# Optimization experiments

Measured on AMD Instinct MI355X. Metric: run time of the kernel, lower is better.

## Reference

```python
import jax, jax.numpy as jnp
import numpy as np

BN_EPS = 1e-5


def setup_inputs() -> dict:
    key = jax.random.key(0)
    ks = jax.random.split(key, 12)
    N, E, H, INV = 100000, 500000, 128, 16
    DIN = 2 * H + INV  # 272
    x_send = jax.random.normal(ks[0], (N, H), dtype=jnp.float32)
    x_rec = jax.random.normal(ks[1], (N, H), dtype=jnp.float32)
    index = jax.random.randint(ks[2], (2, E), 0, N, dtype=jnp.int64)
    edge_attr = jax.random.normal(ks[3], (E, INV), dtype=jnp.float32)
    # message_mlp = BatchNorm1d(272) -> Linear(272,128) -> SiLU  (eval-mode BN)
    bn_gamma = jax.random.normal(ks[4], (DIN,), dtype=jnp.float32) * 0.1 + 1.0
    bn_beta = jax.random.normal(ks[5], (DIN,), dtype=jnp.float32) * 0.1
    bn_mean = jax.random.normal(ks[6], (DIN,), dtype=jnp.float32) * 0.1
    bn_var = jax.random.uniform(ks[7], (DIN,), dtype=jnp.float32) + 0.5
    W1 = jax.random.normal(ks[8], (DIN, H), dtype=jnp.float32) / np.sqrt(DIN)
    b1 = jnp.zeros((H,), dtype=jnp.float32)
    # edge_inf_mlp = Linear(128,1) -> Sigmoid
    W2 = jax.random.normal(ks[9], (H, 1), dtype=jnp.float32) / np.sqrt(H)
    b2 = jnp.zeros((1,), dtype=jnp.float32)
    return {"x_send": x_send, "x_rec": x_rec, "index": index, "edge_attr": edge_attr,
            "bn_gamma": bn_gamma, "bn_beta": bn_beta, "bn_mean": bn_mean, "bn_var": bn_var,
            "W1": W1, "b1": b1, "W2": W2, "b2": b2}


def reference(x_send, x_rec, index, edge_attr, bn_gamma, bn_beta, bn_mean, bn_var, W1, b1, W2, b2):
    idx_send, idx_rec = index[0], index[1]
    # gather + concat -> [E, 2H + INV]
    state = jnp.concatenate((x_send[idx_send], x_rec[idx_rec], edge_attr), axis=1)
    # eval-mode BatchNorm1d
    state = (state - bn_mean) * (bn_gamma * jax.lax.rsqrt(bn_var + BN_EPS)) + bn_beta
    # Linear + SiLU
    messages = jax.nn.silu(state @ W1 + b1)  # [E, H]
    # edge gating: Linear(H,1) + Sigmoid
    edge_weights = jax.nn.sigmoid(messages @ W2 + b2)  # [E, 1]
    # scatter_add aggregation over receiving nodes
    return jax.ops.segment_sum(messages * edge_weights, idx_rec, num_segments=x_rec.shape[0])
```

## Files before the change

kernel.cpp:

```cpp
#include <hip/hip_runtime.h>
#include <hip/hip_bf16.h>
#include <hip/hip_fp16.h>
#include <math.h>

#define HDIM 128
#define INVD 16
#define DIN 272
#define NKT 9

typedef __attribute__((ext_vector_type(4))) float f32x4;
typedef __attribute__((ext_vector_type(4))) unsigned u32x4;
typedef __attribute__((ext_vector_type(8))) short bf16x8;
typedef __attribute__((ext_vector_type(2))) __fp16 fp16x2;

__device__ inline short f2bf(float f) {
    union { float f; unsigned u; } v; v.f = f;
    unsigned r = v.u + 0x7FFFu + ((v.u >> 16) & 1u);
    return (short)(r >> 16);
}

__device__ inline unsigned cvt_pk_bf16(float a, float b) {
    unsigned r;
    asm("v_cvt_pk_bf16_f32 %0, %1, %2" : "=v"(r) : "v"(a), "v"(b));
    return r;
}

__device__ inline float fast_rcp(float x) {
    float r;
    asm("v_rcp_f32 %0, %1" : "=v"(r) : "v"(x));
    return r;
}

__global__ __launch_bounds__(256) void tobf16_kernel(const float* __restrict__ in,
                                                     unsigned short* __restrict__ o,
                                                     int n) {
    int i = (blockIdx.x * 256 + threadIdx.x) * 8;
    if (i < n) {
        f32x4 a = *(const f32x4*)(in + i);
        f32x4 b = *(const f32x4*)(in + i + 4);
        u32x4 r;
        r[0] = cvt_pk_bf16(a[0], a[1]);
        r[1] = cvt_pk_bf16(a[2], a[3]);
        r[2] = cvt_pk_bf16(b[0], b[1]);
        r[3] = cvt_pk_bf16(b[2], b[3]);
        *(u32x4*)(o + i) = r;
    }
}

template<int MODE>
__global__ __launch_bounds__(256, 2) void etnn_kernel(
    const float* __restrict__ x_send,
    const float* __restrict__ x_rec,
    const int*   __restrict__ index,
    const float* __restrict__ edge_attr,
    const float* __restrict__ bn_gamma,
    const float* __restrict__ bn_beta,
    const float* __restrict__ bn_mean,
    const float* __restrict__ bn_var,
    const float* __restrict__ W1,
    const float* __restrict__ b1,
    const float* __restrict__ W2,
    const float* __restrict__ b2,
    const unsigned short* __restrict__ xsb,
    const unsigned short* __restrict__ xrb,
    float* __restrict__ out,
    __half* __restrict__ ws,
    int E, int nIter)
{
    __shared__ short btab[NKT * 8 * 64 * 8];
    __shared__ float scl[DIN];
    __shared__ float shf[DIN];
    __shared__ float bias2[2][HDIM];
    __shared__ float biasT[HDIM];

    const int tid = threadIdx.x;
    const int l  = tid & 63;
    const int lr = l & 15;
    const int lg = l >> 4;

    for (int c = tid; c < DIN; c += 256) {
        float sc = bn_gamma[c] * rsqrtf(bn_var[c] + 1e-5f);
        scl[c] = sc;
        shf[c] = bn_beta[c] - bn_mean[c] * sc;
    }
    __syncthreads();

    for (int f = tid; f < NKT * 8 * 64; f += 256) {
        const int kk  = f >> 9;
        const int cb  = (f >> 6) & 7;
        const int ln  = f & 63;
        const int k0  = kk * 32 + (ln >> 4) * 8;
        const int col = cb * 16 + (ln & 15);
        bf16x8 bv;
        #pragma unroll
        for (int j = 0; j < 8; ++j) {
            const int k = k0 + j;
            float v = (k < DIN) ? scl[k] * W1[k * HDIM + col] : 0.f;
            bv[j] = f2bf(v);
        }
        *(bf16x8*)&btab[f * 8] = bv;
    }
    {
        const int col  = tid & 127;
        const int half = tid >> 7;
        float s = 0.f;
        for (int k = half * 136; k < half * 136 + 136; ++k)
            s += shf[k] * W1[k * HDIM + col];
        bias2[half][col] = s;
    }
    __syncthreads();
    if (tid < HDIM) biasT[tid] = b1[tid] + bias2[0][tid] + bias2[1][tid];
    __syncthreads();

    float biasv[8], w2v[8];
    #pragma unroll
    for (int cb = 0; cb < 8; ++cb) {
        biasv[cb] = biasT[cb * 16 + lr];
        w2v[cb]   = W2[cb * 16 + lr];
    }
    const float b2v = b2[0];
    const bool evn = !(lr & 1);

    const int gw = blockIdx.x * 4 + (tid >> 6);
    const int NW = gridDim.x * 4;

    if (gw >= nIter) return;

    int pc, is, ir;
    {
        int pos = gw * 16 + lr;
        pc = (pos < E) ? pos : E - 1;
        is = index[pc];
        ir = index[E + pc];
    }

    for (int it = gw; it < nIter; it += NW) {
        const int e0 = it * 16;

        bf16x8 Hs[4], Hr[4];
        f32x4  La[2];
        f32x4  LsF[8], LrF[8];

        if constexpr (MODE == 1) {
            const bf16x8* ps = (const bf16x8*)(xsb + (size_t)is * HDIM);
            const bf16x8* pr = (const bf16x8*)(xrb + (size_t)ir * HDIM);
            #pragma unroll
            for (int kk = 0; kk < 4; ++kk) {
                Hs[kk] = ps[kk * 4 + lg];
                Hr[kk] = pr[kk * 4 + lg];
            }
            if (lg < 2) {
                const f32x4* pa = (const f32x4*)(edge_attr + (size_t)pc * INVD + lg * 8);
                La[0] = pa[0]; La[1] = pa[1];
            } else {
                La[0] = (f32x4){0.f, 0.f, 0.f, 0.f};
                La[1] = (f32x4){0.f, 0.f, 0.f, 0.f};
            }
        } else {
            const f32x4* ps = (const f32x4*)(x_send + (size_t)is * HDIM);
            const f32x4* pr = (const f32x4*)(x_rec  + (size_t)ir * HDIM);
            #pragma unroll
            for (int kk = 0; kk < 4; ++kk) {
                LsF[kk * 2]     = ps[kk * 8 + lg * 2];
                LsF[kk * 2 + 1] = ps[kk * 8 + lg * 2 + 1];
                LrF[kk * 2]     = pr[kk * 8 + lg * 2];
                LrF[kk * 2 + 1] = pr[kk * 8 + lg * 2 + 1];
            }
            if (lg < 2) {
                const f32x4* pa = (const f32x4*)(edge_attr + (size_t)pc * INVD + lg * 8);
                La[0] = pa[0]; La[1] = pa[1];
            } else {
                La[0] = (f32x4){0.f, 0.f, 0.f, 0.f};
                La[1] = (f32x4){0.f, 0.f, 0.f, 0.f};
            }
        }

        const int irc = ir;
        {
            int itn = it + NW;
            int pos = (itn < nIter) ? itn * 16 + lr : pc;
            int pcn = (pos < E) ? pos : E - 1;
            pc = pcn;
            is = index[pcn];
            ir = index[E + pcn];
        }

        if constexpr (MODE == 1) {
            asm volatile("" :
                "+v"(Hs[0]), "+v"(Hs[1]), "+v"(Hs[2]), "+v"(Hs[3]),
                "+v"(Hr[0]), "+v"(Hr[1]), "+v"(Hr[2]), "+v"(Hr[3]),
                "+v"(La[0]), "+v"(La[1]));
        }

        f32x4 acc[8];
        #pragma unroll
        for (int cb = 0; cb < 8; ++cb) acc[cb] = (f32x4){0.f, 0.f, 0.f, 0.f};

        #pragma unroll
        for (int kk = 0; kk < NKT; ++kk) {
            union { bf16x8 v; unsigned u[4]; } a;
            if constexpr (MODE == 1) {
                if (kk < 4)       a.v = Hs[kk];
                else if (kk < 8)  a.v = Hr[kk - 4];
                else {
                    a.u[0] = cvt_pk_bf16(La[0][0], La[0][1]);
                    a.u[1] = cvt_pk_bf16(La[0][2], La[0][3]);
                    a.u[2] = cvt_pk_bf16(La[1][0], La[1][1]);
                    a.u[3] = cvt_pk_bf16(La[1][2], La[1][3]);
                }
            } else {
                f32x4 lo = (kk < 4) ? LsF[kk * 2]     : (kk < 8) ? LrF[(kk - 4) * 2]     : La[0];
                f32x4 hi = (kk < 4) ? LsF[kk * 2 + 1] : (kk < 8) ? LrF[(kk - 4) * 2 + 1] : La[1];
                a.u[0] = cvt_pk_bf16(lo[0], lo[1]);
                a.u[1] = cvt_pk_bf16(lo[2], lo[3]);
                a.u[2] = cvt_pk_bf16(hi[0], hi[1]);
                a.u[3] = cvt_pk_bf16(hi[2], hi[3]);
            }
            #pragma unroll
            for (int cb = 0; cb < 8; ++cb) {
                bf16x8 b = *(const bf16x8*)&btab[((kk * 8 + cb) * 64 + l) * 8];
                acc[cb] = __builtin_amdgcn_mfma_f32_16x16x32_bf16(a.v, b, acc[cb], 0, 0, 0);
            }
        }

        float p[4] = {0.f, 0.f, 0.f, 0.f};
        #pragma unroll
        for (int cb = 0; cb < 8; ++cb) {
            #pragma unroll
            for (int q = 0; q < 4; ++q) {
                float z = acc[cb][q] + biasv[cb];
                float m = z * fast_rcp(1.f + __expf(-z));
                acc[cb][q] = m;
                p[q] += m * w2v[cb];
            }
        }
        #pragma unroll
        for (int q = 0; q < 4; ++q) {
            p[q] += __shfl_xor(p[q], 1, 64);
            p[q] += __shfl_xor(p[q], 2, 64);
            p[q] += __shfl_xor(p[q], 4, 64);
            p[q] += __shfl_xor(p[q], 8, 64);
        }

        #pragma unroll
        for (int q = 0; q < 4; ++q) {
            const int row = lg * 4 + q;
            if (e0 + row < E) {
                const int irq = __shfl(irc, row, 64);
                const float g = fast_rcp(1.f + __expf(-(p[q] + b2v)));
                if constexpr (MODE == 1) {
                    float m[8];
                    #pragma unroll
                    for (int cb = 0; cb < 8; ++cb) m[cb] = acc[cb][q] * g;
                    #pragma unroll
                    for (int c = 0; c < 4; ++c) {
                        float x0 = __shfl_xor(m[2 * c],     1, 64);
                        float x1 = __shfl_xor(m[2 * c + 1], 1, 64);
                        float va = evn ? m[2 * c] : x1;
                        float vb = evn ? x0       : m[2 * c + 1];
                        union { fp16x2 h; unsigned u; } pk;
                        pk.h = __builtin_amdgcn_cvt_pkrtz(va, vb);
                        const int col0 = evn ? (32 * c + lr) : (32 * c + 15 + lr);
                        unsigned long long a =
                            (unsigned long long)(ws + (size_t)irq * HDIM + col0);
                        asm volatile("global_atomic_pk_add_f16 %0, %1, off"
                                     :: "v"(a), "v"(pk.u) : "memory");
                    }
                } else {
                    float* orow = out + (size_t)irq * HDIM + lr;
                    #pragma unroll
                    for (int cb = 0; cb < 8; ++cb)
                        atomicAdd(orow + cb * 16, acc[cb][q] * g);
                }
            }
        }
    }
}

__global__ __launch_bounds__(256) void cvt_kernel(const __half* __restrict__ ws,
                                                  float* __restrict__ out, int n) {
    int i = (blockIdx.x * 256 + threadIdx.x) * 4;
    if (i < n) {
        const __half2* p = (const __half2*)(ws + i);
        float2 a = __half22float2(p[0]);
        float2 b = __half22float2(p[1]);
        f32x4 v = {a.x, a.y, b.x, b.y};
        *(f32x4*)(out + i) = v;
    }
}

extern "C" void kernel_launch(void* const* d_in, const int* in_sizes, int n_in,
                              void* d_out, int out_size, void* d_ws, size_t ws_size,
                              hipStream_t stream) {
    const float* x_send    = (const float*)d_in[0];
    const float* x_rec     = (const float*)d_in[1];
    const int*   index     = (const int*)d_in[2];
    const float* edge_attr = (const float*)d_in[3];
    const float* bn_gamma  = (const float*)d_in[4];
    const float* bn_beta   = (const float*)d_in[5];
    const float* bn_mean   = (const float*)d_in[6];
    const float* bn_var    = (const float*)d_in[7];
    const float* W1        = (const float*)d_in[8];
    const float* b1        = (const float*)d_in[9];
    const float* W2        = (const float*)d_in[10];
    const float* b2        = (const float*)d_in[11];
    float* out = (float*)d_out;

    const int E = in_sizes[3] / INVD;
    const int N = in_sizes[0] / HDIM;
    const int nIter = (E + 15) / 16;
    const int grid = 512;
    const int nElem = N * HDIM;

    const size_t accBytes = (size_t)nElem * sizeof(__half);
    const size_t accAl    = (accBytes + 255) & ~(size_t)255;
    const size_t bfBytes  = (size_t)nElem * sizeof(unsigned short);
    const size_t bfAl     = (bfBytes + 255) & ~(size_t)255;

    if (ws_size >= accAl + 2 * bfAl) {
        __half* ws = (__half*)d_ws;
        unsigned short* xsb = (unsigned short*)((char*)d_ws + accAl);
        unsigned short* xrb = (unsigned short*)((char*)d_ws + accAl + bfAl);
        hipMemsetAsync(ws, 0, accBytes, stream);
        const int cb = (nElem / 8 + 255) / 256;
        tobf16_kernel<<<cb, 256, 0, stream>>>(x_send, xsb, nElem);
        tobf16_kernel<<<cb, 256, 0, stream>>>(x_rec,  xrb, nElem);
        etnn_kernel<1><<<grid, 256, 0, stream>>>(x_send, x_rec, index, edge_attr,
                                                 bn_gamma, bn_beta, bn_mean, bn_var,
                                                 W1, b1, W2, b2, xsb, xrb,
                                                 out, ws, E, nIter);
        cvt_kernel<<<(nElem / 4 + 255) / 256, 256, 0, stream>>>(ws, out, nElem);
    } else {
        hipMemsetAsync(d_out, 0, (size_t)out_size * sizeof(float), stream);
        etnn_kernel<0><<<grid, 256, 0, stream>>>(x_send, x_rec, index, edge_attr,
                                                 bn_gamma, bn_beta, bn_mean, bn_var,
                                                 W1, b1, W2, b2, nullptr, nullptr,
                                                 out, nullptr, E, nIter);
    }
}
```

Baseline: 226.0 us.

## Precompute packed BN-folded W1 once in a prep kernel, read from global

Moves the BN folding and bf16 packing of W1 out of every block into a single-block prep kernel that writes the packed weights and fused bias to workspace. The main kernel now reads B fragments from global/L2 instead of LDS, which removes per-block setup and frees shared memory. The grid grows from 512 to 2048 blocks, and the asm barrier that pinned the prefetched registers is dropped. In exchange, B operand loads become global loads inside the MFMA loop, and the fallback path assumes the workspace can hold the pack.

```diff
diff --git a/kernel.cpp b/kernel.cpp
--- a/kernel.cpp
+++ b/kernel.cpp
@@ -7,6 +7,7 @@
 #define INVD 16
 #define DIN 272
 #define NKT 9
+#define PACKSH (NKT * 8 * 64 * 8)
 
 typedef __attribute__((ext_vector_type(4))) float f32x4;
 typedef __attribute__((ext_vector_type(4))) unsigned u32x4;
@@ -47,36 +48,16 @@
     }
 }
 
-template<int MODE>
-__global__ __launch_bounds__(256, 2) void etnn_kernel(
-    const float* __restrict__ x_send,
-    const float* __restrict__ x_rec,
-    const int*   __restrict__ index,
-    const float* __restrict__ edge_attr,
-    const float* __restrict__ bn_gamma,
-    const float* __restrict__ bn_beta,
-    const float* __restrict__ bn_mean,
-    const float* __restrict__ bn_var,
-    const float* __restrict__ W1,
-    const float* __restrict__ b1,
-    const float* __restrict__ W2,
-    const float* __restrict__ b2,
-    const unsigned short* __restrict__ xsb,
-    const unsigned short* __restrict__ xrb,
-    float* __restrict__ out,
-    __half* __restrict__ ws,
-    int E, int nIter)
+__global__ __launch_bounds__(256) void prep_kernel(
+    const float* __restrict__ bn_gamma, const float* __restrict__ bn_beta,
+    const float* __restrict__ bn_mean,  const float* __restrict__ bn_var,
+    const float* __restrict__ W1,       const float* __restrict__ b1,
+    short* __restrict__ W1pack, float* __restrict__ biasTg)
 {
-    __shared__ short btab[NKT * 8 * 64 * 8];
     __shared__ float scl[DIN];
     __shared__ float shf[DIN];
     __shared__ float bias2[2][HDIM];
-    __shared__ float biasT[HDIM];
-
     const int tid = threadIdx.x;
-    const int l  = tid & 63;
-    const int lr = l & 15;
-    const int lg = l >> 4;
 
     for (int c = tid; c < DIN; c += 256) {
         float sc = bn_gamma[c] * rsqrtf(bn_var[c] + 1e-5f);
@@ -98,7 +79,7 @@
             float v = (k < DIN) ? scl[k] * W1[k * HDIM + col] : 0.f;
             bv[j] = f2bf(v);
         }
-        *(bf16x8*)&btab[f * 8] = bv;
+        *(bf16x8*)&W1pack[f * 8] = bv;
     }
     {
         const int col  = tid & 127;
@@ -109,13 +90,34 @@
         bias2[half][col] = s;
     }
     __syncthreads();
-    if (tid < HDIM) biasT[tid] = b1[tid] + bias2[0][tid] + bias2[1][tid];
-    __syncthreads();
+    if (tid < HDIM) biasTg[tid] = b1[tid] + bias2[0][tid] + bias2[1][tid];
+}
+
+template<int MODE>
+__global__ __launch_bounds__(256, 2) void etnn_kernel(
+    const float* __restrict__ x_send,
+    const float* __restrict__ x_rec,
+    const int*   __restrict__ index,
+    const float* __restrict__ edge_attr,
+    const float* __restrict__ W2,
+    const float* __restrict__ b2,
+    const short* __restrict__ W1pack,
+    const float* __restrict__ biasTg,
+    const unsigned short* __restrict__ xsb,
+    const unsigned short* __restrict__ xrb,
+    float* __restrict__ out,
+    __half* __restrict__ ws,
+    int E, int nIter)
+{
+    const int tid = threadIdx.x;
+    const int l  = tid & 63;
+    const int lr = l & 15;
+    const int lg = l >> 4;
 
     float biasv[8], w2v[8];
     #pragma unroll
     for (int cb = 0; cb < 8; ++cb) {
-        biasv[cb] = biasT[cb * 16 + lr];
+        biasv[cb] = biasTg[cb * 16 + lr];
         w2v[cb]   = W2[cb * 16 + lr];
     }
     const float b2v = b2[0];
@@ -183,13 +185,6 @@
             pc = pcn;
             is = index[pcn];
             ir = index[E + pcn];
-        }
-
-        if constexpr (MODE == 1) {
-            asm volatile("" :
-                "+v"(Hs[0]), "+v"(Hs[1]), "+v"(Hs[2]), "+v"(Hs[3]),
-                "+v"(Hr[0]), "+v"(Hr[1]), "+v"(Hr[2]), "+v"(Hr[3]),
-                "+v"(La[0]), "+v"(La[1]));
         }
 
         f32x4 acc[8];
@@ -218,7 +213,7 @@
             }
             #pragma unroll
             for (int cb = 0; cb < 8; ++cb) {
-                bf16x8 b = *(const bf16x8*)&btab[((kk * 8 + cb) * 64 + l) * 8];
+                bf16x8 b = *(const bf16x8*)&W1pack[((kk * 8 + cb) * 64 + l) * 8];
                 acc[cb] = __builtin_amdgcn_mfma_f32_16x16x32_bf16(a.v, b, acc[cb], 0, 0, 0);
             }
         }
@@ -309,32 +304,40 @@
     const int E = in_sizes[3] / INVD;
     const int N = in_sizes[0] / HDIM;
     const int nIter = (E + 15) / 16;
-    const int grid = 512;
+    const int grid = 2048;
     const int nElem = N * HDIM;
 
-    const size_t accBytes = (size_t)nElem * sizeof(__half);
-    const size_t accAl    = (accBytes + 255) & ~(size_t)255;
-    const size_t bfBytes  = (size_t)nElem * sizeof(unsigned short);
-    const size_t bfAl     = (bfBytes + 255) & ~(size_t)255;
-
-    if (ws_size >= accAl + 2 * bfAl) {
+    const size_t accBytes  = (size_t)nElem * sizeof(__half);
+    const size_t accAl     = (accBytes + 255) & ~(size_t)255;
+    const size_t bfBytes   = (size_t)nElem * sizeof(unsigned short);
+    const size_t bfAl      = (bfBytes + 255) & ~(size_t)255;
+    const size_t packBytes = (size_t)PACKSH * sizeof(short) + HDIM * sizeof(float);
+    const size_t packAl    = (packBytes + 255) & ~(size_t)255;
+
+    if (ws_size >= accAl + 2 * bfAl + packAl) {
         __half* ws = (__half*)d_ws;
         unsigned short* xsb = (unsigned short*)((char*)d_ws + accAl);
         unsigned short* xrb = (unsigned short*)((char*)d_ws + accAl + bfAl);
+        short* pack  = (short*)((char*)d_ws + accAl + 2 * bfAl);
+        float* biasg = (float*)(pack + PACKSH);
         hipMemsetAsync(ws, 0, accBytes, stream);
         const int cb = (nElem / 8 + 255) / 256;
         tobf16_kernel<<<cb, 256, 0, stream>>>(x_send, xsb, nElem);
         tobf16_kernel<<<cb, 256, 0, stream>>>(x_rec,  xrb, nElem);
+        prep_kernel<<<1, 256, 0, stream>>>(bn_gamma, bn_beta, bn_mean, bn_var,
+                                           W1, b1, pack, biasg);
         etnn_kernel<1><<<grid, 256, 0, stream>>>(x_send, x_rec, index, edge_attr,
-                                                 bn_gamma, bn_beta, bn_mean, bn_var,
-                                                 W1, b1, W2, b2, xsb, xrb,
+                                                 W2, b2, pack, biasg, xsb, xrb,
                                                  out, ws, E, nIter);
         cvt_kernel<<<(nElem / 4 + 255) / 256, 256, 0, stream>>>(ws, out, nElem);
     } else {
+        short* pack  = (short*)d_ws;
+        float* biasg = (float*)(pack + PACKSH);
         hipMemsetAsync(d_out, 0, (size_t)out_size * sizeof(float), stream);
+        prep_kernel<<<1, 256, 0, stream>>>(bn_gamma, bn_beta, bn_mean, bn_var,
+                                           W1, b1, pack, biasg);
         etnn_kernel<0><<<grid, 256, 0, stream>>>(x_send, x_rec, index, edge_attr,
-                                                 bn_gamma, bn_beta, bn_mean, bn_var,
-                                                 W1, b1, W2, b2, nullptr, nullptr,
+                                                 W2, b2, pack, biasg, nullptr, nullptr,
                                                  out, nullptr, E, nIter);
     }
 }
```

After: 464.5 us. 2.06x slower.

## Double-buffer bf16 feature gathers to overlap next tile's loads with MFMA compute

Applied to the files above, without the earlier changes.

In the bf16 (MODE 1) path, the loop now keeps two register buffers (A/B) of gathered sender/receiver rows and edge attributes. It issues the gather for the next tile before computing the current one, and prefetches indices two tiles ahead. The goal is to hide the latency of the random-row global loads behind MFMA and epilogue work. The cost is roughly double the VGPRs held live for gathered data, which may lower occupancy. The fp32 path is only restructured and keeps the same behavior.

```diff
diff --git a/kernel.cpp b/kernel.cpp
--- a/kernel.cpp
+++ b/kernel.cpp
@@ -126,22 +126,16 @@
 
     if (gw >= nIter) return;
 
-    int pc, is, ir;
-    {
-        int pos = gw * 16 + lr;
-        pc = (pos < E) ? pos : E - 1;
+    auto ldIdx = [&](int itx, int& pc, int& is, int& ir) {
+        int pos = itx * 16 + lr;
+        pc = (pos < E && pos >= 0) ? pos : E - 1;
         is = index[pc];
         ir = index[E + pc];
-    }
-
-    for (int it = gw; it < nIter; it += NW) {
-        const int e0 = it * 16;
-
-        bf16x8 Hs[4], Hr[4];
-        f32x4  La[2];
-        f32x4  LsF[8], LrF[8];
-
-        if constexpr (MODE == 1) {
+    };
+
+    if constexpr (MODE == 1) {
+        auto issueGather = [&](int pc, int is, int ir,
+                               bf16x8* Hs, bf16x8* Hr, f32x4* La) {
             const bf16x8* ps = (const bf16x8*)(xsb + (size_t)is * HDIM);
             const bf16x8* pr = (const bf16x8*)(xrb + (size_t)ir * HDIM);
             #pragma unroll
@@ -156,50 +150,17 @@
                 La[0] = (f32x4){0.f, 0.f, 0.f, 0.f};
                 La[1] = (f32x4){0.f, 0.f, 0.f, 0.f};
             }
-        } else {
-            const f32x4* ps = (const f32x4*)(x_send + (size_t)is * HDIM);
-            const f32x4* pr = (const f32x4*)(x_rec  + (size_t)ir * HDIM);
-            #pragma unroll
-            for (int kk = 0; kk < 4; ++kk) {
-                LsF[kk * 2]     = ps[kk * 8 + lg * 2];
-                LsF[kk * 2 + 1] = ps[kk * 8 + lg * 2 + 1];
-                LrF[kk * 2]     = pr[kk * 8 + lg * 2];
-                LrF[kk * 2 + 1] = pr[kk * 8 + lg * 2 + 1];
-            }
-            if (lg < 2) {
-                const f32x4* pa = (const f32x4*)(edge_attr + (size_t)pc * INVD + lg * 8);
-                La[0] = pa[0]; La[1] = pa[1];
-            } else {
-                La[0] = (f32x4){0.f, 0.f, 0.f, 0.f};
-                La[1] = (f32x4){0.f, 0.f, 0.f, 0.f};
-            }
-        }
-
-        const int irc = ir;
-        {
-            int itn = it + NW;
-            int pos = (itn < nIter) ? itn * 16 + lr : pc;
-            int pcn = (pos < E) ? pos : E - 1;
-            pc = pcn;
-            is = index[pcn];
-            ir = index[E + pcn];
-        }
-
-        if constexpr (MODE == 1) {
-            asm volatile("" :
-                "+v"(Hs[0]), "+v"(Hs[1]), "+v"(Hs[2]), "+v"(Hs[3]),
-                "+v"(Hr[0]), "+v"(Hr[1]), "+v"(Hr[2]), "+v"(Hr[3]),
-                "+v"(La[0]), "+v"(La[1]));
-        }
-
-        f32x4 acc[8];
-        #pragma unroll
-        for (int cb = 0; cb < 8; ++cb) acc[cb] = (f32x4){0.f, 0.f, 0.f, 0.f};
-
-        #pragma unroll
-        for (int kk = 0; kk < NKT; ++kk) {
-            union { bf16x8 v; unsigned u[4]; } a;
-            if constexpr (MODE == 1) {
+        };
+
+        auto computeTile = [&](int e0, int irc,
+                               bf16x8* Hs, bf16x8* Hr, f32x4* La) {
+            f32x4 acc[8];
+            #pragma unroll
+            for (int cb = 0; cb < 8; ++cb) acc[cb] = (f32x4){0.f, 0.f, 0.f, 0.f};
+
+            #pragma unroll
+            for (int kk = 0; kk < NKT; ++kk) {
+                union { bf16x8 v; unsigned u[4]; } a;
                 if (kk < 4)       a.v = Hs[kk];
                 else if (kk < 8)  a.v = Hr[kk - 4];
                 else {
@@ -208,47 +169,38 @@
                     a.u[2] = cvt_pk_bf16(La[1][0], La[1][1]);
                     a.u[3] = cvt_pk_bf16(La[1][2], La[1][3]);
                 }
-            } else {
-                f32x4 lo = (kk < 4) ? LsF[kk * 2]     : (kk < 8) ? LrF[(kk - 4) * 2]     : La[0];
-                f32x4 hi = (kk < 4) ? LsF[kk * 2 + 1] : (kk < 8) ? LrF[(kk - 4) * 2 + 1] : La[1];
-                a.u[0] = cvt_pk_bf16(lo[0], lo[1]);
-                a.u[1] = cvt_pk_bf16(lo[2], lo[3]);
-                a.u[2] = cvt_pk_bf16(hi[0], hi[1]);
-                a.u[3] = cvt_pk_bf16(hi[2], hi[3]);
-            }
+                #pragma unroll
+                for (int cb = 0; cb < 8; ++cb) {
+                    bf16x8 b = *(const bf16x8*)&btab[((kk * 8 + cb) * 64 + l) * 8];
+                    acc[cb] = __builtin_amdgcn_mfma_f32_16x16x32_bf16(a.v, b, acc[cb], 0, 0, 0);
+                }
+            }
+
+            float p[4] = {0.f, 0.f, 0.f, 0.f};
             #pragma unroll
             for (int cb = 0; cb < 8; ++cb) {
-                bf16x8 b = *(const bf16x8*)&btab[((kk * 8 + cb) * 64 + l) * 8];
-                acc[cb] = __builtin_amdgcn_mfma_f32_16x16x32_bf16(a.v, b, acc[cb], 0, 0, 0);
-            }
-        }
-
-        float p[4] = {0.f, 0.f, 0.f, 0.f};
-        #pragma unroll
-        for (int cb = 0; cb < 8; ++cb) {
+                #pragma unroll
+                for (int q = 0; q < 4; ++q) {
+                    float z = acc[cb][q] + biasv[cb];
+                    float m = z * fast_rcp(1.f + __expf(-z));
+                    acc[cb][q] = m;
+                    p[q] += m * w2v[cb];
+                }
+            }
             #pragma unroll
             for (int q = 0; q < 4; ++q) {
-                float z = acc[cb][q] + biasv[cb];
-                float m = z * fast_rcp(1.f + __expf(-z));
-                acc[cb][q] = m;
-                p[q] += m * w2v[cb];
-            }
-        }
-        #pragma unroll
-        for (int q = 0; q < 4; ++q) {
-            p[q] += __shfl_xor(p[q], 1, 64);
-            p[q] += __shfl_xor(p[q], 2, 64);
-            p[q] += __shfl_xor(p[q], 4, 64);
-            p[q] += __shfl_xor(p[q], 8, 64);
-        }
-
-        #pragma unroll
-        for (int q = 0; q < 4; ++q) {
-            const int row = lg * 4 + q;
-            if (e0 + row < E) {
-                const int irq = __shfl(irc, row, 64);
-                const float g = fast_rcp(1.f + __expf(-(p[q] + b2v)));
-                if constexpr (MODE == 1) {
+                p[q] += __shfl_xor(p[q], 1, 64);
+                p[q] += __shfl_xor(p[q], 2, 64);
+                p[q] += __shfl_xor(p[q], 4, 64);
+                p[q] += __shfl_xor(p[q], 8, 64);
+            }
+
+            #pragma unroll
+            for (int q = 0; q < 4; ++q) {
+                const int row = lg * 4 + q;
+                if (e0 + row < E) {
+                    const int irq = __shfl(irc, row, 64);
+                    const float g = fast_rcp(1.f + __expf(-(p[q] + b2v)));
                     float m[8];
                     #pragma unroll
                     for (int cb = 0; cb < 8; ++cb) m[cb] = acc[cb][q] * g;
@@ -266,7 +218,113 @@
                         asm volatile("global_atomic_pk_add_f16 %0, %1, off"
                                      :: "v"(a), "v"(pk.u) : "memory");
                     }
-                } else {
+                }
+            }
+        };
+
+        bf16x8 HsA[4], HrA[4]; f32x4 LaA[2];
+        bf16x8 HsB[4], HrB[4]; f32x4 LaB[2];
+
+        int pc0, is0, ir0, pc1, is1, ir1;
+        ldIdx(gw, pc0, is0, ir0);
+        issueGather(pc0, is0, ir0, HsA, HrA, LaA);
+        ldIdx(gw + NW, pc1, is1, ir1);
+
+        for (int it = gw; it < nIter; it += 2 * NW) {
+            issueGather(pc1, is1, ir1, HsB, HrB, LaB);
+            int pc2, is2, ir2;
+            ldIdx(it + 2 * NW, pc2, is2, ir2);
+            asm volatile("" :
+                "+v"(HsB[0]), "+v"(HsB[1]), "+v"(HsB[2]), "+v"(HsB[3]),
+                "+v"(HrB[0]), "+v"(HrB[1]), "+v"(HrB[2]), "+v"(HrB[3]),
+                "+v"(LaB[0]), "+v"(LaB[1]));
+            computeTile(it * 16, ir0, HsA, HrA, LaA);
+
+            issueGather(pc2, is2, ir2, HsA, HrA, LaA);
+            int pc3, is3, ir3;
+            ldIdx(it + 3 * NW, pc3, is3, ir3);
+            asm volatile("" :
+                "+v"(HsA[0]), "+v"(HsA[1]), "+v"(HsA[2]), "+v"(HsA[3]),
+                "+v"(HrA[0]), "+v"(HrA[1]), "+v"(HrA[2]), "+v"(HrA[3]),
+                "+v"(LaA[0]), "+v"(LaA[1]));
+            if (it + NW < nIter)
+                computeTile((it + NW) * 16, ir1, HsB, HrB, LaB);
+
+            pc0 = pc2; is0 = is2; ir0 = ir2;
+            pc1 = pc3; is1 = is3; ir1 = ir3;
+        }
+    } else {
+        int pc, is, ir;
+        ldIdx(gw, pc, is, ir);
+        for (int it = gw; it < nIter; it += NW) {
+            const int e0 = it * 16;
+            const f32x4* ps = (const f32x4*)(x_send + (size_t)is * HDIM);
+            const f32x4* pr = (const f32x4*)(x_rec  + (size_t)ir * HDIM);
+            f32x4 LsF[8], LrF[8], La[2];
+            #pragma unroll
+            for (int kk = 0; kk < 4; ++kk) {
+                LsF[kk * 2]     = ps[kk * 8 + lg * 2];
+                LsF[kk * 2 + 1] = ps[kk * 8 + lg * 2 + 1];
+                LrF[kk * 2]     = pr[kk * 8 + lg * 2];
+                LrF[kk * 2 + 1] = pr[kk * 8 + lg * 2 + 1];
+            }
+            if (lg < 2) {
+                const f32x4* pa = (const f32x4*)(edge_attr + (size_t)pc * INVD + lg * 8);
+                La[0] = pa[0]; La[1] = pa[1];
+            } else {
+                La[0] = (f32x4){0.f, 0.f, 0.f, 0.f};
+                La[1] = (f32x4){0.f, 0.f, 0.f, 0.f};
+            }
+            const int irc = ir;
+            {
+                int itn = it + NW;
+                int pos = (itn < nIter) ? itn * 16 + lr : pc;
+                int pcn = (pos < E) ? pos : E - 1;
+                pc = pcn; is = index[pcn]; ir = index[E + pcn];
+            }
+
+            f32x4 acc[8];
+            #pragma unroll
+            for (int cb = 0; cb < 8; ++cb) acc[cb] = (f32x4){0.f, 0.f, 0.f, 0.f};
+            #pragma unroll
+            for (int kk = 0; kk < NKT; ++kk) {
+                f32x4 lo = (kk < 4) ? LsF[kk * 2]     : (kk < 8) ? LrF[(kk - 4) * 2]     : La[0];
+                f32x4 hi = (kk < 4) ? LsF[kk * 2 + 1] : (kk < 8) ? LrF[(kk - 4) * 2 + 1] : La[1];
+                union { bf16x8 v; unsigned u[4]; } a;
+                a.u[0] = cvt_pk_bf16(lo[0], lo[1]);
+                a.u[1] = cvt_pk_bf16(lo[2], lo[3]);
+                a.u[2] = cvt_pk_bf16(hi[0], hi[1]);
+                a.u[3] = cvt_pk_bf16(hi[2], hi[3]);
+                #pragma unroll
+                for (int cb = 0; cb < 8; ++cb) {
+                    bf16x8 b = *(const bf16x8*)&btab[((kk * 8 + cb) * 64 + l) * 8];
+                    acc[cb] = __builtin_amdgcn_mfma_f32_16x16x32_bf16(a.v, b, acc[cb], 0, 0, 0);
+                }
+            }
+            float p[4] = {0.f, 0.f, 0.f, 0.f};
+            #pragma unroll
+            for (int cb = 0; cb < 8; ++cb) {
+                #pragma unroll
+                for (int q = 0; q < 4; ++q) {
+                    float z = acc[cb][q] + biasv[cb];
+                    float m = z * fast_rcp(1.f + __expf(-z));
+                    acc[cb][q] = m;
+                    p[q] += m * w2v[cb];
+                }
+            }
+            #pragma unroll
+            for (int q = 0; q < 4; ++q) {
+                p[q] += __shfl_xor(p[q], 1, 64);
+                p[q] += __shfl_xor(p[q], 2, 64);
+                p[q] += __shfl_xor(p[q], 4, 64);
+                p[q] += __shfl_xor(p[q], 8, 64);
+            }
+            #pragma unroll
+            for (int q = 0; q < 4; ++q) {
+                const int row = lg * 4 + q;
+                if (e0 + row < E) {
+                    const int irq = __shfl(irc, row, 64);
+                    const float g = fast_rcp(1.f + __expf(-(p[q] + b2v)));
                     float* orow = out + (size_t)irq * HDIM + lr;
                     #pragma unroll
                     for (int cb = 0; cb < 8; ++cb)
```

New measurement: 229.4 us. Within noise of the previous version (+1.5%).
